# Kernel tuning notes

Measured on AMD Instinct MI355X. Metric: run time of the kernel, lower is better.

## Reference

```python
import jax, jax.numpy as jnp
import numpy as np
from jax import lax

B, C, H, W = 4, 64, 64, 64
CH = C // 2  # edge_detect hidden channels
BN_EPS = 1e-5


def conv1x1(x, w, b):
    # x: (B,C,H,W), w: (O,C), b: (O,)
    return jnp.einsum('bchw,oc->bohw', x, w) + b[None, :, None, None]


def setup_inputs() -> dict:
    key = jax.random.key(0)
    ks = jax.random.split(key, 12)
    s = 1.0 / np.sqrt(C)
    inp = {
        'x': jax.random.normal(ks[0], (B, C, H, W), jnp.float32),
        'Wq': jax.random.normal(ks[1], (C, C), jnp.float32) * s,
        'bq': jnp.zeros((C,), jnp.float32),
        'Wk': jax.random.normal(ks[2], (C, C), jnp.float32) * s,
        'bk': jnp.zeros((C,), jnp.float32),
        'Wv': jax.random.normal(ks[3], (C, C), jnp.float32) * s,
        'bv': jnp.zeros((C,), jnp.float32),
        'We1': jax.random.normal(ks[4], (CH, C, 3, 3), jnp.float32) * (1.0 / np.sqrt(C * 9)),
        'be1': jnp.zeros((CH,), jnp.float32),
        'bn_w': jnp.ones((CH,), jnp.float32),
        'bn_b': jnp.zeros((CH,), jnp.float32),
        'bn_mean': jnp.zeros((CH,), jnp.float32),
        'bn_var': jnp.ones((CH,), jnp.float32),
        'We2': jax.random.normal(ks[5], (1, CH), jnp.float32) * (1.0 / np.sqrt(CH)),
        'be2': jnp.zeros((1,), jnp.float32),
        'gamma': jax.random.normal(ks[6], (1,), jnp.float32) * 0.1,
        'beta': jax.random.normal(ks[7], (1,), jnp.float32) * 0.1,
    }
    return inp


def reference(x, Wq, bq, Wk, bk, Wv, bv, We1, be1, bn_w, bn_b, bn_mean, bn_var, We2, be2, gamma, beta):
    b, c, h, w = x.shape
    hw = h * w
    q = conv1x1(x, Wq, bq).reshape(b, c, hw).transpose(0, 2, 1)  # (B,HW,C)
    k = conv1x1(x, Wk, bk).reshape(b, c, hw)                      # (B,C,HW)
    v = conv1x1(x, Wv, bv).reshape(b, c, hw)                      # (B,C,HW)

    energy = jnp.einsum('bnc,bcm->bnm', q, k)                      # (B,HW,HW)
    attention = jax.nn.softmax(energy, axis=-1)

    # edge_detect: 3x3 conv -> BN (eval stats) -> ReLU -> 1x1 conv -> sigmoid
    e = lax.conv_general_dilated(x, We1, (1, 1), 'SAME',
                                 dimension_numbers=('NCHW', 'OIHW', 'NCHW'))
    e = e + be1[None, :, None, None]
    e = (e - bn_mean[None, :, None, None]) * jax.lax.rsqrt(bn_var + BN_EPS)[None, :, None, None]
    e = e * bn_w[None, :, None, None] + bn_b[None, :, None, None]
    e = jax.nn.relu(e)
    e = conv1x1(e, We2, be2)                                       # (B,1,H,W)
    edge = jax.nn.sigmoid(e).reshape(b, 1, hw)                     # (B,1,HW)

    fa = attention * (1.0 + beta[0] * edge)                        # broadcast over query dim
    denom = jnp.maximum(jnp.sum(jnp.abs(fa), axis=2, keepdims=True), 1e-12)
    fa = fa / denom                                                # L1 renorm along keys

    out = jnp.einsum('bcm,bnm->bcn', v, fa).reshape(b, c, h, w)
    return gamma[0] * out + x
```

## Files before the change

### kernel.cpp

```cpp
#include <hip/hip_runtime.h>
#include <hip/hip_bf16.h>

typedef unsigned short u16;
typedef __attribute__((ext_vector_type(8))) __bf16 bf16x8;
typedef __attribute__((ext_vector_type(4))) float f32x4;


#define NSPLIT 4

__device__ __forceinline__ u16 f2bf(float f) {
    unsigned u = __builtin_bit_cast(unsigned, f);
    u += 0x7FFFu + ((u >> 16) & 1u);
    return (u16)(u >> 16);
}
__device__ __forceinline__ float bf2f(u16 v) {
    unsigned u = ((unsigned)v) << 16;
    return __builtin_bit_cast(float, u);
}

__global__ __launch_bounds__(256) void qkv_edge_kernel(
    const float* __restrict__ x,
    const float* __restrict__ Wq, const float* __restrict__ bq,
    const float* __restrict__ Wk, const float* __restrict__ bk,
    const float* __restrict__ Wv, const float* __restrict__ bv,
    const float* __restrict__ We1, const float* __restrict__ be1,
    const float* __restrict__ bn_w, const float* __restrict__ bn_b,
    const float* __restrict__ bn_mean, const float* __restrict__ bn_var,
    const float* __restrict__ We2, const float* __restrict__ be2,
    const float* __restrict__ beta,
    u16* __restrict__ Qt, u16* __restrict__ Kt, u16* __restrict__ Vm,
    float* __restrict__ wkey)
{
    __shared__ __align__(16) u16 sm[33280];
    const int t = threadIdx.x;
    const int wv = t >> 6, lane = t & 63;
    const int quad = lane >> 4, l15 = lane & 15;

    if (blockIdx.x < 256) {
        u16* Wl   = sm;
        u16* xt_s = sm + 13824;
        u16* vt   = sm + 13824 + 4224;
        const int b = blockIdx.x >> 6;
        const int n0 = (blockIdx.x & 63) << 6;

        const float* Wmat[3] = {Wq, Wk, Wv};
#pragma unroll
        for (int m = 0; m < 3; ++m)
#pragma unroll
            for (int i = 0; i < 4; ++i) {
                int u = t + i * 256;
                float4 w4 = *reinterpret_cast<const float4*>(Wmat[m] + u * 4);
                int row = u >> 4, col = (u & 15) * 4;
                uint2 pk;
                pk.x = (unsigned)f2bf(w4.x) | ((unsigned)f2bf(w4.y) << 16);
                pk.y = (unsigned)f2bf(w4.z) | ((unsigned)f2bf(w4.w) << 16);
                *reinterpret_cast<uint2*>(&Wl[(m * 64 + row) * 72 + col]) = pk;
            }
        for (int i = 0; i < 16; ++i) {
            int lin = t + i * 256;
            int c = lin >> 6, nn = lin & 63;
            xt_s[nn * 66 + c] = f2bf(x[(size_t)(b * 64 + c) * 4096 + n0 + nn]);
        }
        __syncthreads();

        bf16x8 bx[2];
#pragma unroll
        for (int h = 0; h < 2; ++h)
            bx[h] = *reinterpret_cast<const bf16x8*>(
                &xt_s[(wv * 16 + l15) * 66 + h * 32 + quad * 8]);

        f32x4 d[3][4];
#pragma unroll
        for (int m = 0; m < 3; ++m)
#pragma unroll
            for (int mt = 0; mt < 4; ++mt) d[m][mt] = (f32x4){0.f, 0.f, 0.f, 0.f};

#pragma unroll
        for (int h = 0; h < 2; ++h)
#pragma unroll
            for (int m = 0; m < 3; ++m)
#pragma unroll
                for (int mt = 0; mt < 4; ++mt) {
                    bf16x8 af = *reinterpret_cast<const bf16x8*>(
                        &Wl[(m * 64 + mt * 16 + l15) * 72 + h * 32 + quad * 8]);
                    d[m][mt] = __builtin_amdgcn_mfma_f32_16x16x32_bf16(af, bx[h], d[m][mt], 0, 0, 0);
                }

        const float* bias[3] = {bq, bk, bv};
        const float L2E = 1.44269504f;
#pragma unroll
        for (int m = 0; m < 3; ++m)
#pragma unroll
            for (int mt = 0; mt < 4; ++mt) {
                float4 bi = *reinterpret_cast<const float4*>(bias[m] + mt * 16 + quad * 4);
                d[m][mt][0] += bi.x; d[m][mt][1] += bi.y; d[m][mt][2] += bi.z; d[m][mt][3] += bi.w;
                if (m == 0) {
                    d[m][mt][0] *= L2E; d[m][mt][1] *= L2E;
                    d[m][mt][2] *= L2E; d[m][mt][3] *= L2E;
                }
            }

        const int rowchunk = (n0 >> 4) + wv;
#pragma unroll
        for (int m = 0; m < 2; ++m) {
            u16* base = (m == 0 ? Qt : Kt) + (size_t)b * 262144;
#pragma unroll
            for (int mt = 0; mt < 4; ++mt) {
                uint2 pk;
                pk.x = (unsigned)f2bf(d[m][mt][0]) | ((unsigned)f2bf(d[m][mt][1]) << 16);
                pk.y = (unsigned)f2bf(d[m][mt][2]) | ((unsigned)f2bf(d[m][mt][3]) << 16);
                *reinterpret_cast<uint2*>(
                    base + ((size_t)(rowchunk * 8 + mt * 2 + (quad >> 1))) * 128 +
                    l15 * 8 + (quad & 1) * 4) = pk;
            }
        }
#pragma unroll
        for (int mt = 0; mt < 4; ++mt)
#pragma unroll
            for (int r = 0; r < 4; ++r)
                vt[(mt * 16 + quad * 4 + r) * 72 + wv * 16 + l15] = f2bf(d[2][mt][r]);
        __syncthreads();
        {
            u16* Vb_st = Vm + (size_t)b * 262144;
            const int kt = n0 >> 6;
#pragma unroll
            for (int i = 0; i < 2; ++i) {
                int unit = t + i * 256;
                int f = unit >> 7, hq = (unit >> 4) & 7, cl = unit & 15;
                const u16* src = &vt[(f * 16 + cl) * 72 + hq * 8];
                uint4 v4 = *reinterpret_cast<const uint4*>(src);
                *reinterpret_cast<uint4*>(
                    Vb_st + ((size_t)((kt * 4 + f) * 8 + hq)) * 128 + cl * 8) = v4;
            }
        }
    } else {
        u16* Ae_s = sm;
        u16* xr_s = sm + 18688;
        const int eb = blockIdx.x - 256;
        const int b = eb >> 6, h = eb & 63;

        if (t < 192) {
            int kh = t / 64, rem = t & 63;
            int col = (rem >> 5) * 65, ci2 = (rem & 31) * 2;
            *reinterpret_cast<unsigned*>(&xr_s[(kh * 66 + col) * 72 + ci2]) = 0u;
        }
#pragma unroll
        for (int i = 0; i < 18; ++i) {
            int u = t + i * 256;
            int ch = u / 144;
            int rem = u - ch * 144;
            int p = rem >> 4, cig = (rem & 15) * 4;
            const float* src = We1 + ch * 576 + cig * 9 + p;
            float a = src[0], b2 = src[9], c2 = src[18], d2 = src[27];
            uint2 pk;
            pk.x = (unsigned)f2bf(a) | ((unsigned)f2bf(b2) << 16);
            pk.y = (unsigned)f2bf(c2) | ((unsigned)f2bf(d2) << 16);
            *reinterpret_cast<uint2*>(&Ae_s[ch * 584 + p * 64 + cig]) = pk;
        }
#pragma unroll
        for (int i = 0; i < 12; ++i) {
            int u = t + i * 256;
            int w = u & 63, cig = (u >> 6) & 15, kh = u >> 10;
            int hs = h + kh - 1;
            float v0 = 0.f, v1 = 0.f, v2 = 0.f, v3 = 0.f;
            if ((unsigned)hs < 64u) {
                const float* src = x + ((size_t)(b * 64 + cig * 4) * 64 + hs) * 64 + w;
                v0 = src[0]; v1 = src[4096]; v2 = src[8192]; v3 = src[12288];
            }
            uint2 pk;
            pk.x = (unsigned)f2bf(v0) | ((unsigned)f2bf(v1) << 16);
            pk.y = (unsigned)f2bf(v2) | ((unsigned)f2bf(v3) << 16);
            *reinterpret_cast<uint2*>(&xr_s[(kh * 66 + w + 1) * 72 + cig * 4]) = pk;
        }
        __syncthreads();

        f32x4 e[2];
        e[0] = (f32x4){0.f, 0.f, 0.f, 0.f};
        e[1] = (f32x4){0.f, 0.f, 0.f, 0.f};
#pragma unroll
        for (int p = 0; p < 9; ++p) {
            const int kh = p / 3, kw = p - kh * 3;
#pragma unroll
            for (int half = 0; half < 2; ++half) {
                bf16x8 bfr = *reinterpret_cast<const bf16x8*>(
                    &xr_s[(kh * 66 + wv * 16 + l15 + kw) * 72 + half * 32 + quad * 8]);
#pragma unroll
                for (int mt = 0; mt < 2; ++mt) {
                    bf16x8 af = *reinterpret_cast<const bf16x8*>(
                        &Ae_s[(mt * 16 + l15) * 584 + p * 64 + half * 32 + quad * 8]);
                    e[mt] = __builtin_amdgcn_mfma_f32_16x16x32_bf16(af, bfr, e[mt], 0, 0, 0);
                }
            }
        }
        float partial = 0.f;
#pragma unroll
        for (int mt = 0; mt < 2; ++mt) {
            float4 bw = *reinterpret_cast<const float4*>(bn_w    + mt * 16 + quad * 4);
            float4 bb = *reinterpret_cast<const float4*>(bn_b    + mt * 16 + quad * 4);
            float4 bm = *reinterpret_cast<const float4*>(bn_mean + mt * 16 + quad * 4);
            float4 bv2 = *reinterpret_cast<const float4*>(bn_var + mt * 16 + quad * 4);
            float4 b1 = *reinterpret_cast<const float4*>(be1     + mt * 16 + quad * 4);
            float4 w2 = *reinterpret_cast<const float4*>(We2     + mt * 16 + quad * 4);
            float sc, sh;
            sc = bw.x * rsqrtf(bv2.x + 1e-5f); sh = (b1.x - bm.x) * sc + bb.x;
            partial += fmaxf(e[mt][0] * sc + sh, 0.f) * w2.x;
            sc = bw.y * rsqrtf(bv2.y + 1e-5f); sh = (b1.y - bm.y) * sc + bb.y;
            partial += fmaxf(e[mt][1] * sc + sh, 0.f) * w2.y;
            sc = bw.z * rsqrtf(bv2.z + 1e-5f); sh = (b1.z - bm.z) * sc + bb.z;
            partial += fmaxf(e[mt][2] * sc + sh, 0.f) * w2.z;
            sc = bw.w * rsqrtf(bv2.w + 1e-5f); sh = (b1.w - bm.w) * sc + bb.w;
            partial += fmaxf(e[mt][3] * sc + sh, 0.f) * w2.w;
        }
        partial += __shfl_xor(partial, 16);
        partial += __shfl_xor(partial, 32);
        if (lane < 16) {
            float s = partial + be2[0];
            float sg = 1.f / (1.f + __expf(-s));
            wkey[(size_t)b * 4096 + h * 64 + wv * 16 + lane] = 1.f + beta[0] * sg;
        }
    }
}

__global__ __launch_bounds__(128, 2) void attn_kernel(
    const u16* __restrict__ Qt, const u16* __restrict__ Kt,
    const u16* __restrict__ Vm, const float* __restrict__ wkey,
    u16* __restrict__ O_part, float* __restrict__ l_part)
{
    constexpr int KT_ITERS = 64 / NSPLIT;
    const int t = threadIdx.x;
    const int qi = blockIdx.x / NSPLIT;
    const int split = blockIdx.x % NSPLIT;
    const int b = qi >> 6;
    const int n0 = (qi & 63) << 6;
    const int wv = t >> 6, lane = t & 63;
    const int quad = lane >> 4, l15 = lane & 15;

    const int src0 = ((quad & 1) * 2) * 16 + l15;
    const int src1 = src0 + 16;
    const bool msel = (quad >> 1) != 0;

    const u16* Qb = Qt + (size_t)b * 262144;
    const u16* Kb = Kt + (size_t)b * 262144;
    const u16* Vb = Vm + (size_t)b * 262144;
    const float* wb = wkey + (size_t)b * 4096;

    bf16x8 qf[2][2];
#pragma unroll
    for (int nt = 0; nt < 2; ++nt)
#pragma unroll
        for (int h = 0; h < 2; ++h)
            qf[nt][h] = __builtin_bit_cast(bf16x8, *reinterpret_cast<const uint4*>(
                Qb + ((size_t)(((n0 >> 4) + wv * 2 + nt) * 8 + h * 4 + quad)) * 128 + l15 * 8));

    const int kt0 = split * KT_ITERS;
    uint4 kf[4][2];
    float4 wf[4];
#pragma unroll
    for (int mt = 0; mt < 4; ++mt) {
#pragma unroll
        for (int h = 0; h < 2; ++h)
            kf[mt][h] = *reinterpret_cast<const uint4*>(
                Kb + ((size_t)((kt0 * 4 + mt) * 8 + h * 4 + quad)) * 128 + l15 * 8);
        wf[mt] = *reinterpret_cast<const float4*>(wb + kt0 * 64 + mt * 16 + quad * 4);
    }

    const uint4 ones_u = {0x3F803F80u, 0x3F803F80u, 0x3F803F80u, 0x3F803F80u};
    const bf16x8 onesf = __builtin_bit_cast(bf16x8, ones_u);

    f32x4 o[4][2];
    f32x4 l5[2];
#pragma unroll
    for (int fc = 0; fc < 4; ++fc)
#pragma unroll
        for (int nt = 0; nt < 2; ++nt) o[fc][nt] = (f32x4){0.f, 0.f, 0.f, 0.f};
#pragma unroll
    for (int nt = 0; nt < 2; ++nt) l5[nt] = (f32x4){0.f, 0.f, 0.f, 0.f};

    for (int kt = kt0; kt < kt0 + KT_ITERS; ++kt) {
        uint4 vf[4][2];
#pragma unroll
        for (int f = 0; f < 4; ++f)
#pragma unroll
            for (int h = 0; h < 2; ++h)
                vf[f][h] = *reinterpret_cast<const uint4*>(
                    Vb + ((size_t)((kt * 4 + f) * 8 + h * 4 + quad)) * 128 + l15 * 8);

        f32x4 s[4][2];
#pragma unroll
        for (int mt = 0; mt < 4; ++mt)
#pragma unroll
            for (int nt = 0; nt < 2; ++nt) {
                f32x4 a = (f32x4){0.f, 0.f, 0.f, 0.f};
                a = __builtin_amdgcn_mfma_f32_16x16x32_bf16(
                        __builtin_bit_cast(bf16x8, kf[mt][0]), qf[nt][0], a, 0, 0, 0);
                a = __builtin_amdgcn_mfma_f32_16x16x32_bf16(
                        __builtin_bit_cast(bf16x8, kf[mt][1]), qf[nt][1], a, 0, 0, 0);
                s[mt][nt] = a;
            }

        const int ktn = (kt + 1 < kt0 + KT_ITERS) ? kt + 1 : kt0;
#pragma unroll
        for (int mt = 0; mt < 4; ++mt)
#pragma unroll
            for (int h = 0; h < 2; ++h)
                kf[mt][h] = *reinterpret_cast<const uint4*>(
                    Kb + ((size_t)((ktn * 4 + mt) * 8 + h * 4 + quad)) * 128 + l15 * 8);

        uint2 pk[4][2];
        const float OFF = 17.3123405f;
#pragma unroll
        for (int mt = 0; mt < 4; ++mt) {
            const float* wfp = reinterpret_cast<const float*>(&wf[mt]);
#pragma unroll
            for (int nt = 0; nt < 2; ++nt) {
                float p0 = exp2f(s[mt][nt][0] - OFF) * wfp[0];
                float p1 = exp2f(s[mt][nt][1] - OFF) * wfp[1];
                float p2 = exp2f(s[mt][nt][2] - OFF) * wfp[2];
                float p3 = exp2f(s[mt][nt][3] - OFF) * wfp[3];
                unsigned u0 = __builtin_bit_cast(unsigned, p0);
                unsigned u1 = __builtin_bit_cast(unsigned, p1);
                unsigned u2 = __builtin_bit_cast(unsigned, p2);
                unsigned u3 = __builtin_bit_cast(unsigned, p3);
                pk[mt][nt].x = (u0 >> 16) | (u1 & 0xFFFF0000u);
                pk[mt][nt].y = (u2 >> 16) | (u3 & 0xFFFF0000u);
            }
        }

#pragma unroll
        for (int mt = 0; mt < 4; ++mt)
            wf[mt] = *reinterpret_cast<const float4*>(wb + ktn * 64 + mt * 16 + quad * 4);

        bf16x8 pb[2][2];
#pragma unroll
        for (int h = 0; h < 2; ++h)
#pragma unroll
            for (int nt = 0; nt < 2; ++nt) {
                unsigned a0x = (unsigned)__shfl((int)pk[h * 2][nt].x, src0, 64);
                unsigned a1x = (unsigned)__shfl((int)pk[h * 2 + 1][nt].x, src0, 64);
                unsigned a0y = (unsigned)__shfl((int)pk[h * 2][nt].y, src0, 64);
                unsigned a1y = (unsigned)__shfl((int)pk[h * 2 + 1][nt].y, src0, 64);
                unsigned a0z = (unsigned)__shfl((int)pk[h * 2][nt].x, src1, 64);
                unsigned a1z = (unsigned)__shfl((int)pk[h * 2 + 1][nt].x, src1, 64);
                unsigned a0w = (unsigned)__shfl((int)pk[h * 2][nt].y, src1, 64);
                unsigned a1w = (unsigned)__shfl((int)pk[h * 2 + 1][nt].y, src1, 64);
                uint4 g;
                g.x = msel ? a1x : a0x;
                g.y = msel ? a1y : a0y;
                g.z = msel ? a1z : a0z;
                g.w = msel ? a1w : a0w;
                pb[nt][h] = __builtin_bit_cast(bf16x8, g);
            }

#pragma unroll
        for (int nt = 0; nt < 2; ++nt) {
#pragma unroll
            for (int fc = 0; fc < 4; ++fc) {
                o[fc][nt] = __builtin_amdgcn_mfma_f32_16x16x32_bf16(
                    __builtin_bit_cast(bf16x8, vf[fc][0]), pb[nt][0], o[fc][nt], 0, 0, 0);
                o[fc][nt] = __builtin_amdgcn_mfma_f32_16x16x32_bf16(
                    __builtin_bit_cast(bf16x8, vf[fc][1]), pb[nt][1], o[fc][nt], 0, 0, 0);
            }
            l5[nt] = __builtin_amdgcn_mfma_f32_16x16x32_bf16(onesf, pb[nt][0], l5[nt], 0, 0, 0);
            l5[nt] = __builtin_amdgcn_mfma_f32_16x16x32_bf16(onesf, pb[nt][1], l5[nt], 0, 0, 0);
        }
    }

    const size_t pbase = (size_t)blockIdx.x * 4096;
#pragma unroll
    for (int nt = 0; nt < 2; ++nt) {
        if (quad == 0)
            l_part[(size_t)blockIdx.x * 64 + wv * 32 + nt * 16 + l15] = l5[nt][0];
#pragma unroll
        for (int fc = 0; fc < 4; ++fc) {
            uint2 pk2;
            pk2.x = (unsigned)f2bf(o[fc][nt][0]) | ((unsigned)f2bf(o[fc][nt][1]) << 16);
            pk2.y = (unsigned)f2bf(o[fc][nt][2]) | ((unsigned)f2bf(o[fc][nt][3]) << 16);
            *reinterpret_cast<uint2*>(
                &O_part[pbase + ((((wv * 2 + nt) * 4 + fc) * 4 + quad)) * 64 + l15 * 4]) = pk2;
        }
    }
}

__global__ __launch_bounds__(256) void combine_kernel(
    const u16* __restrict__ O_part, const float* __restrict__ l_part,
    const float* __restrict__ x, const float* __restrict__ g_gamma,
    float* __restrict__ out)
{
    __shared__ float ot[16 * 68];
    __shared__ float ls[16];
    const int t = threadIdx.x;
    const int qi = blockIdx.x >> 2;
    const int quarter = blockIdx.x & 3;
    const int b = qi >> 6;
    const int n0 = (qi & 63) << 6;
    const int rbase = (quarter >> 1) * 32 + (quarter & 1) * 16;
    const int f = t >> 6, quad = (t >> 4) & 3, l15 = t & 15;
    const float gamma = g_gamma[0];

    {
        float a0 = 0.f, a1 = 0.f, a2 = 0.f, a3 = 0.f;
#pragma unroll
        for (int s4 = 0; s4 < NSPLIT; ++s4) {
            const u16* base = O_part + ((size_t)(qi * NSPLIT + s4)) * 4096;
            uint2 u = *reinterpret_cast<const uint2*>(
                base + (((quarter * 4 + f) * 4 + quad)) * 64 + l15 * 4);
            a0 += bf2f((u16)(u.x & 0xFFFF));
            a1 += bf2f((u16)(u.x >> 16));
            a2 += bf2f((u16)(u.y & 0xFFFF));
            a3 += bf2f((u16)(u.y >> 16));
        }
        float4 v4; v4.x = a0; v4.y = a1; v4.z = a2; v4.w = a3;
        *reinterpret_cast<float4*>(&ot[l15 * 68 + f * 16 + quad * 4]) = v4;
        if (t < 16) {
            float lsum = 0.f;
#pragma unroll
            for (int s4 = 0; s4 < NSPLIT; ++s4)
                lsum += l_part[((size_t)(qi * NSPLIT + s4)) * 64 + rbase + t];
            ls[t] = gamma / fmaxf(lsum, 1e-30f);
        }
    }
    __syncthreads();
    {
        const int c = t >> 2, nseg = t & 3;
        const size_t gbase = ((size_t)(b * 64 + c)) * 4096 + n0 + rbase + nseg * 4;
        float4 xv = *reinterpret_cast<const float4*>(&x[gbase]);
        float4 rv;
        int nl = nseg * 4;
        rv.x = ot[(nl + 0) * 68 + c] * ls[nl + 0] + xv.x;
        rv.y = ot[(nl + 1) * 68 + c] * ls[nl + 1] + xv.y;
        rv.z = ot[(nl + 2) * 68 + c] * ls[nl + 2] + xv.z;
        rv.w = ot[(nl + 3) * 68 + c] * ls[nl + 3] + xv.w;
        *reinterpret_cast<float4*>(&out[gbase]) = rv;
    }
}

extern "C" void kernel_launch(void* const* d_in, const int* in_sizes, int n_in,
                              void* d_out, int out_size, void* d_ws, size_t ws_size,
                              hipStream_t stream) {
    const float* x      = (const float*)d_in[0];
    const float* Wq     = (const float*)d_in[1];
    const float* bq     = (const float*)d_in[2];
    const float* Wk     = (const float*)d_in[3];
    const float* bk     = (const float*)d_in[4];
    const float* Wv     = (const float*)d_in[5];
    const float* bv     = (const float*)d_in[6];
    const float* We1    = (const float*)d_in[7];
    const float* be1    = (const float*)d_in[8];
    const float* bn_w   = (const float*)d_in[9];
    const float* bn_b   = (const float*)d_in[10];
    const float* bn_mean= (const float*)d_in[11];
    const float* bn_var = (const float*)d_in[12];
    const float* We2    = (const float*)d_in[13];
    const float* be2    = (const float*)d_in[14];
    const float* gamma  = (const float*)d_in[15];
    const float* beta   = (const float*)d_in[16];

    char* ws = (char*)d_ws;
    const size_t KB = 1024, MB = 1024 * 1024;
    u16*   Qt     = (u16*)ws;
    u16*   Kt     = (u16*)(ws + 2 * MB);
    u16*   Vm     = (u16*)(ws + 4 * MB);
    float* wkey   = (float*)(ws + 6 * MB);
    float* l_part = (float*)(ws + 6 * MB + 64 * KB);
    u16*   O_part = (u16*)(ws + 6 * MB + 576 * KB);

    float* out = (float*)d_out;

    qkv_edge_kernel<<<dim3(512), dim3(256), 0, stream>>>(
        x, Wq, bq, Wk, bk, Wv, bv, We1, be1, bn_w, bn_b, bn_mean, bn_var,
        We2, be2, beta, Qt, Kt, Vm, wkey);
    attn_kernel<<<dim3(256 * NSPLIT), dim3(128), 0, stream>>>(
        Qt, Kt, Vm, wkey, O_part, l_part);
    combine_kernel<<<dim3(1024), dim3(256), 0, stream>>>(
        O_part, l_part, x, gamma, out);
}
```

Before: 138.8 us.

## Switch attention to 32x32x16 MFMA with log-weight fold and permlane swap

Rewrites the attention kernel around 32x32x16 bf16 MFMA tiles with 256-thread blocks, each covering 128 queries. The edge weight is now stored as log2 with the offset folded in, so the kernel does one add inside exp2 instead of a subtract and a multiply. The row sum is accumulated in scalar registers instead of with an extra ones-MFMA. P is packed with the hardware cvt_pk_bf16 instruction and rearranged with permlane32_swap instead of eight shuffles per fragment. The combine kernel and output layout change to match, with fewer blocks overall and possibly higher register pressure.

Measured after the change: 156.4 us. +12.7%, slower.

```diff
diff --git a/kernel.cpp b/kernel.cpp
--- a/kernel.cpp
+++ b/kernel.cpp
@@ -4,6 +4,7 @@
 typedef unsigned short u16;
 typedef __attribute__((ext_vector_type(8))) __bf16 bf16x8;
 typedef __attribute__((ext_vector_type(4))) float f32x4;
+typedef __attribute__((ext_vector_type(16))) float f32x16;
 
 
 #define NSPLIT 4
@@ -216,169 +217,155 @@
         if (lane < 16) {
             float s = partial + be2[0];
             float sg = 1.f / (1.f + __expf(-s));
-            wkey[(size_t)b * 4096 + h * 64 + wv * 16 + lane] = 1.f + beta[0] * sg;
+            wkey[(size_t)b * 4096 + h * 64 + wv * 16 + lane] =
+                __log2f(fmaxf(1.f + beta[0] * sg, 1e-20f)) - 17.3123405f;
         }
     }
 }
 
-__global__ __launch_bounds__(128, 2) void attn_kernel(
+__global__ __launch_bounds__(256, 2) void attn_kernel(
     const u16* __restrict__ Qt, const u16* __restrict__ Kt,
-    const u16* __restrict__ Vm, const float* __restrict__ wkey,
+    const u16* __restrict__ Vm, const float* __restrict__ lwkey,
     u16* __restrict__ O_part, float* __restrict__ l_part)
 {
     constexpr int KT_ITERS = 64 / NSPLIT;
     const int t = threadIdx.x;
     const int qi = blockIdx.x / NSPLIT;
     const int split = blockIdx.x % NSPLIT;
-    const int b = qi >> 6;
-    const int n0 = (qi & 63) << 6;
+    const int b = qi >> 5;
+    const int n0 = (qi & 31) << 7;
     const int wv = t >> 6, lane = t & 63;
-    const int quad = lane >> 4, l15 = lane & 15;
-
-    const int src0 = ((quad & 1) * 2) * 16 + l15;
-    const int src1 = src0 + 16;
-    const bool msel = (quad >> 1) != 0;
+    const int l31 = lane & 31, hi = lane >> 5;
+    const int i4 = (lane >> 4) & 1, l15 = lane & 15;
 
     const u16* Qb = Qt + (size_t)b * 262144;
     const u16* Kb = Kt + (size_t)b * 262144;
     const u16* Vb = Vm + (size_t)b * 262144;
-    const float* wb = wkey + (size_t)b * 4096;
-
-    bf16x8 qf[2][2];
-#pragma unroll
-    for (int nt = 0; nt < 2; ++nt)
-#pragma unroll
-        for (int h = 0; h < 2; ++h)
-            qf[nt][h] = __builtin_bit_cast(bf16x8, *reinterpret_cast<const uint4*>(
-                Qb + ((size_t)(((n0 >> 4) + wv * 2 + nt) * 8 + h * 4 + quad)) * 128 + l15 * 8));
+    const float* lwb = lwkey + (size_t)b * 4096;
+
+    bf16x8 qf[4];
+#pragma unroll
+    for (int kc = 0; kc < 4; ++kc)
+        qf[kc] = __builtin_bit_cast(bf16x8, *reinterpret_cast<const uint4*>(
+            Qb + (size_t)(((n0 >> 4) + wv * 2 + i4) * 8 + kc * 2 + hi) * 128 + l15 * 8));
 
     const int kt0 = split * KT_ITERS;
-    uint4 kf[4][2];
-    float4 wf[4];
-#pragma unroll
-    for (int mt = 0; mt < 4; ++mt) {
-#pragma unroll
-        for (int h = 0; h < 2; ++h)
-            kf[mt][h] = *reinterpret_cast<const uint4*>(
-                Kb + ((size_t)((kt0 * 4 + mt) * 8 + h * 4 + quad)) * 128 + l15 * 8);
-        wf[mt] = *reinterpret_cast<const float4*>(wb + kt0 * 64 + mt * 16 + quad * 4);
+    uint4 kf[2][4];
+#pragma unroll
+    for (int tl = 0; tl < 2; ++tl)
+#pragma unroll
+        for (int kc = 0; kc < 4; ++kc)
+            kf[tl][kc] = *reinterpret_cast<const uint4*>(
+                Kb + (size_t)((kt0 * 4 + tl * 2 + i4) * 8 + kc * 2 + hi) * 128 + l15 * 8);
+
+    f32x16 o[2];
+#pragma unroll
+    for (int ct = 0; ct < 2; ++ct)
+#pragma unroll
+        for (int i = 0; i < 16; ++i) o[ct][i] = 0.f;
+    float lacc0 = 0.f, lacc1 = 0.f;
+
+    for (int kt = kt0; kt < kt0 + KT_ITERS; ++kt) {
+        uint4 vf[2][4];
+#pragma unroll
+        for (int ct = 0; ct < 2; ++ct)
+#pragma unroll
+            for (int kc = 0; kc < 4; ++kc)
+                vf[ct][kc] = *reinterpret_cast<const uint4*>(
+                    Vb + (size_t)((kt * 4 + ct * 2 + i4) * 8 + kc * 2 + hi) * 128 + l15 * 8);
+
+        float4 lwv[2][4];
+#pragma unroll
+        for (int tl = 0; tl < 2; ++tl)
+#pragma unroll
+            for (int g = 0; g < 4; ++g)
+                lwv[tl][g] = *reinterpret_cast<const float4*>(
+                    lwb + kt * 64 + tl * 32 + g * 8 + hi * 4);
+
+        f32x16 s[2];
+#pragma unroll
+        for (int tl = 0; tl < 2; ++tl) {
+            f32x16 a;
+#pragma unroll
+            for (int i = 0; i < 16; ++i) a[i] = 0.f;
+#pragma unroll
+            for (int kc = 0; kc < 4; ++kc)
+                a = __builtin_amdgcn_mfma_f32_32x32x16_bf16(
+                        __builtin_bit_cast(bf16x8, kf[tl][kc]), qf[kc], a, 0, 0, 0);
+            s[tl] = a;
+        }
+
+        const int ktn = (kt + 1 < kt0 + KT_ITERS) ? kt + 1 : kt0;
+#pragma unroll
+        for (int tl = 0; tl < 2; ++tl)
+#pragma unroll
+            for (int kc = 0; kc < 4; ++kc)
+                kf[tl][kc] = *reinterpret_cast<const uint4*>(
+                    Kb + (size_t)((ktn * 4 + tl * 2 + i4) * 8 + kc * 2 + hi) * 128 + l15 * 8);
+
+        uint4 pb[2][2];
+#pragma unroll
+        for (int tl = 0; tl < 2; ++tl) {
+            float p[16];
+#pragma unroll
+            for (int g = 0; g < 4; ++g) {
+                const float4 lv = lwv[tl][g];
+                p[4 * g + 0] = exp2f(s[tl][4 * g + 0] + lv.x);
+                p[4 * g + 1] = exp2f(s[tl][4 * g + 1] + lv.y);
+                p[4 * g + 2] = exp2f(s[tl][4 * g + 2] + lv.z);
+                p[4 * g + 3] = exp2f(s[tl][4 * g + 3] + lv.w);
+                lacc0 += p[4 * g + 0] + p[4 * g + 1];
+                lacc1 += p[4 * g + 2] + p[4 * g + 3];
+            }
+#pragma unroll
+            for (int kc2 = 0; kc2 < 2; ++kc2) {
+                int a0, a1, b0, b1;
+                asm("v_cvt_pk_bf16_f32 %0, %1, %2" : "=v"(a0) : "v"(p[kc2 * 8 + 0]), "v"(p[kc2 * 8 + 1]));
+                asm("v_cvt_pk_bf16_f32 %0, %1, %2" : "=v"(a1) : "v"(p[kc2 * 8 + 2]), "v"(p[kc2 * 8 + 3]));
+                asm("v_cvt_pk_bf16_f32 %0, %1, %2" : "=v"(b0) : "v"(p[kc2 * 8 + 4]), "v"(p[kc2 * 8 + 5]));
+                asm("v_cvt_pk_bf16_f32 %0, %1, %2" : "=v"(b1) : "v"(p[kc2 * 8 + 6]), "v"(p[kc2 * 8 + 7]));
+                auto swA = __builtin_amdgcn_permlane32_swap(a0, b0, false, false);
+                auto swB = __builtin_amdgcn_permlane32_swap(a1, b1, false, false);
+                uint4 fr;
+                fr.x = (unsigned)swA[0];
+                fr.y = (unsigned)swB[0];
+                fr.z = (unsigned)swA[1];
+                fr.w = (unsigned)swB[1];
+                pb[tl][kc2] = fr;
+            }
+        }
+
+#pragma unroll
+        for (int ct = 0; ct < 2; ++ct)
+#pragma unroll
+            for (int tl = 0; tl < 2; ++tl)
+#pragma unroll
+                for (int kc2 = 0; kc2 < 2; ++kc2)
+                    o[ct] = __builtin_amdgcn_mfma_f32_32x32x16_bf16(
+                        __builtin_bit_cast(bf16x8, vf[ct][tl * 2 + kc2]),
+                        __builtin_bit_cast(bf16x8, pb[tl][kc2]), o[ct], 0, 0, 0);
     }
 
-    const uint4 ones_u = {0x3F803F80u, 0x3F803F80u, 0x3F803F80u, 0x3F803F80u};
-    const bf16x8 onesf = __builtin_bit_cast(bf16x8, ones_u);
-
-    f32x4 o[4][2];
-    f32x4 l5[2];
-#pragma unroll
-    for (int fc = 0; fc < 4; ++fc)
-#pragma unroll
-        for (int nt = 0; nt < 2; ++nt) o[fc][nt] = (f32x4){0.f, 0.f, 0.f, 0.f};
-#pragma unroll
-    for (int nt = 0; nt < 2; ++nt) l5[nt] = (f32x4){0.f, 0.f, 0.f, 0.f};
-
-    for (int kt = kt0; kt < kt0 + KT_ITERS; ++kt) {
-        uint4 vf[4][2];
-#pragma unroll
-        for (int f = 0; f < 4; ++f)
-#pragma unroll
-            for (int h = 0; h < 2; ++h)
-                vf[f][h] = *reinterpret_cast<const uint4*>(
-                    Vb + ((size_t)((kt * 4 + f) * 8 + h * 4 + quad)) * 128 + l15 * 8);
-
-        f32x4 s[4][2];
-#pragma unroll
-        for (int mt = 0; mt < 4; ++mt)
-#pragma unroll
-            for (int nt = 0; nt < 2; ++nt) {
-                f32x4 a = (f32x4){0.f, 0.f, 0.f, 0.f};
-                a = __builtin_amdgcn_mfma_f32_16x16x32_bf16(
-                        __builtin_bit_cast(bf16x8, kf[mt][0]), qf[nt][0], a, 0, 0, 0);
-                a = __builtin_amdgcn_mfma_f32_16x16x32_bf16(
-                        __builtin_bit_cast(bf16x8, kf[mt][1]), qf[nt][1], a, 0, 0, 0);
-                s[mt][nt] = a;
-            }
-
-        const int ktn = (kt + 1 < kt0 + KT_ITERS) ? kt + 1 : kt0;
-#pragma unroll
-        for (int mt = 0; mt < 4; ++mt)
-#pragma unroll
-            for (int h = 0; h < 2; ++h)
-                kf[mt][h] = *reinterpret_cast<const uint4*>(
-                    Kb + ((size_t)((ktn * 4 + mt) * 8 + h * 4 + quad)) * 128 + l15 * 8);
-
-        uint2 pk[4][2];
-        const float OFF = 17.3123405f;
-#pragma unroll
-        for (int mt = 0; mt < 4; ++mt) {
-            const float* wfp = reinterpret_cast<const float*>(&wf[mt]);
-#pragma unroll
-            for (int nt = 0; nt < 2; ++nt) {
-                float p0 = exp2f(s[mt][nt][0] - OFF) * wfp[0];
-                float p1 = exp2f(s[mt][nt][1] - OFF) * wfp[1];
-                float p2 = exp2f(s[mt][nt][2] - OFF) * wfp[2];
-                float p3 = exp2f(s[mt][nt][3] - OFF) * wfp[3];
-                unsigned u0 = __builtin_bit_cast(unsigned, p0);
-                unsigned u1 = __builtin_bit_cast(unsigned, p1);
-                unsigned u2 = __builtin_bit_cast(unsigned, p2);
-                unsigned u3 = __builtin_bit_cast(unsigned, p3);
-                pk[mt][nt].x = (u0 >> 16) | (u1 & 0xFFFF0000u);
-                pk[mt][nt].y = (u2 >> 16) | (u3 & 0xFFFF0000u);
-            }
-        }
-
-#pragma unroll
-        for (int mt = 0; mt < 4; ++mt)
-            wf[mt] = *reinterpret_cast<const float4*>(wb + ktn * 64 + mt * 16 + quad * 4);
-
-        bf16x8 pb[2][2];
-#pragma unroll
-        for (int h = 0; h < 2; ++h)
-#pragma unroll
-            for (int nt = 0; nt < 2; ++nt) {
-                unsigned a0x = (unsigned)__shfl((int)pk[h * 2][nt].x, src0, 64);
-                unsigned a1x = (unsigned)__shfl((int)pk[h * 2 + 1][nt].x, src0, 64);
-                unsigned a0y = (unsigned)__shfl((int)pk[h * 2][nt].y, src0, 64);
-                unsigned a1y = (unsigned)__shfl((int)pk[h * 2 + 1][nt].y, src0, 64);
-                unsigned a0z = (unsigned)__shfl((int)pk[h * 2][nt].x, src1, 64);
-                unsigned a1z = (unsigned)__shfl((int)pk[h * 2 + 1][nt].x, src1, 64);
-                unsigned a0w = (unsigned)__shfl((int)pk[h * 2][nt].y, src1, 64);
-                unsigned a1w = (unsigned)__shfl((int)pk[h * 2 + 1][nt].y, src1, 64);
-                uint4 g;
-                g.x = msel ? a1x : a0x;
-                g.y = msel ? a1y : a0y;
-                g.z = msel ? a1z : a0z;
-                g.w = msel ? a1w : a0w;
-                pb[nt][h] = __builtin_bit_cast(bf16x8, g);
-            }
-
-#pragma unroll
-        for (int nt = 0; nt < 2; ++nt) {
-#pragma unroll
-            for (int fc = 0; fc < 4; ++fc) {
-                o[fc][nt] = __builtin_amdgcn_mfma_f32_16x16x32_bf16(
-                    __builtin_bit_cast(bf16x8, vf[fc][0]), pb[nt][0], o[fc][nt], 0, 0, 0);
-                o[fc][nt] = __builtin_amdgcn_mfma_f32_16x16x32_bf16(
-                    __builtin_bit_cast(bf16x8, vf[fc][1]), pb[nt][1], o[fc][nt], 0, 0, 0);
-            }
-            l5[nt] = __builtin_amdgcn_mfma_f32_16x16x32_bf16(onesf, pb[nt][0], l5[nt], 0, 0, 0);
-            l5[nt] = __builtin_amdgcn_mfma_f32_16x16x32_bf16(onesf, pb[nt][1], l5[nt], 0, 0, 0);
-        }
-    }
-
-    const size_t pbase = (size_t)blockIdx.x * 4096;
-#pragma unroll
-    for (int nt = 0; nt < 2; ++nt) {
-        if (quad == 0)
-            l_part[(size_t)blockIdx.x * 64 + wv * 32 + nt * 16 + l15] = l5[nt][0];
-#pragma unroll
-        for (int fc = 0; fc < 4; ++fc) {
+    float lh = lacc0 + lacc1;
+    float ltot = lh + __shfl_xor(lh, 32);
+    if (lane < 32)
+        l_part[(size_t)blockIdx.x * 128 + wv * 32 + lane] = ltot;
+
+    const size_t pbase = (size_t)blockIdx.x * 8192;
+    const int q = wv * 32 + l31;
+#pragma unroll
+    for (int ct = 0; ct < 2; ++ct)
+#pragma unroll
+        for (int g = 0; g < 4; ++g) {
+            int w0, w1;
+            asm("v_cvt_pk_bf16_f32 %0, %1, %2" : "=v"(w0) : "v"(o[ct][4 * g + 0]), "v"(o[ct][4 * g + 1]));
+            asm("v_cvt_pk_bf16_f32 %0, %1, %2" : "=v"(w1) : "v"(o[ct][4 * g + 2]), "v"(o[ct][4 * g + 3]));
             uint2 pk2;
-            pk2.x = (unsigned)f2bf(o[fc][nt][0]) | ((unsigned)f2bf(o[fc][nt][1]) << 16);
-            pk2.y = (unsigned)f2bf(o[fc][nt][2]) | ((unsigned)f2bf(o[fc][nt][3]) << 16);
+            pk2.x = (unsigned)w0;
+            pk2.y = (unsigned)w1;
             *reinterpret_cast<uint2*>(
-                &O_part[pbase + ((((wv * 2 + nt) * 4 + fc) * 4 + quad)) * 64 + l15 * 4]) = pk2;
-        }
-    }
+                &O_part[pbase + (size_t)(ct * 8 + g * 2 + hi) * 512 + q * 4]) = pk2;
+        }
 }
 
 __global__ __launch_bounds__(256) void combine_kernel(
@@ -386,51 +373,57 @@
     const float* __restrict__ x, const float* __restrict__ g_gamma,
     float* __restrict__ out)
 {
-    __shared__ float ot[16 * 68];
-    __shared__ float ls[16];
+    __shared__ float ot[32 * 65];
+    __shared__ float ls[32];
     const int t = threadIdx.x;
-    const int qi = blockIdx.x >> 2;
-    const int quarter = blockIdx.x & 3;
-    const int b = qi >> 6;
-    const int n0 = (qi & 63) << 6;
-    const int rbase = (quarter >> 1) * 32 + (quarter & 1) * 16;
-    const int f = t >> 6, quad = (t >> 4) & 3, l15 = t & 15;
+    const int ab = blockIdx.x >> 2;
+    const int sub = blockIdx.x & 3;
+    const int b = ab >> 5;
+    const int n0 = (ab & 31) << 7;
     const float gamma = g_gamma[0];
 
-    {
+#pragma unroll
+    for (int i = 0; i < 2; ++i) {
+        int idx = t + i * 256;
+        int c4 = idx >> 5, ql = idx & 31;
         float a0 = 0.f, a1 = 0.f, a2 = 0.f, a3 = 0.f;
 #pragma unroll
         for (int s4 = 0; s4 < NSPLIT; ++s4) {
-            const u16* base = O_part + ((size_t)(qi * NSPLIT + s4)) * 4096;
             uint2 u = *reinterpret_cast<const uint2*>(
-                base + (((quarter * 4 + f) * 4 + quad)) * 64 + l15 * 4);
+                O_part + ((size_t)(ab * NSPLIT + s4)) * 8192 +
+                (size_t)c4 * 512 + (sub * 32 + ql) * 4);
             a0 += bf2f((u16)(u.x & 0xFFFF));
             a1 += bf2f((u16)(u.x >> 16));
             a2 += bf2f((u16)(u.y & 0xFFFF));
             a3 += bf2f((u16)(u.y >> 16));
         }
-        float4 v4; v4.x = a0; v4.y = a1; v4.z = a2; v4.w = a3;
-        *reinterpret_cast<float4*>(&ot[l15 * 68 + f * 16 + quad * 4]) = v4;
-        if (t < 16) {
-            float lsum = 0.f;
-#pragma unroll
-            for (int s4 = 0; s4 < NSPLIT; ++s4)
-                lsum += l_part[((size_t)(qi * NSPLIT + s4)) * 64 + rbase + t];
-            ls[t] = gamma / fmaxf(lsum, 1e-30f);
-        }
+        ot[ql * 65 + c4 * 4 + 0] = a0;
+        ot[ql * 65 + c4 * 4 + 1] = a1;
+        ot[ql * 65 + c4 * 4 + 2] = a2;
+        ot[ql * 65 + c4 * 4 + 3] = a3;
+    }
+    if (t < 32) {
+        float lsum = 0.f;
+#pragma unroll
+        for (int s4 = 0; s4 < NSPLIT; ++s4)
+            lsum += l_part[((size_t)(ab * NSPLIT + s4)) * 128 + sub * 32 + t];
+        ls[t] = gamma / fmaxf(lsum, 1e-30f);
     }
     __syncthreads();
     {
-        const int c = t >> 2, nseg = t & 3;
-        const size_t gbase = ((size_t)(b * 64 + c)) * 4096 + n0 + rbase + nseg * 4;
-        float4 xv = *reinterpret_cast<const float4*>(&x[gbase]);
-        float4 rv;
-        int nl = nseg * 4;
-        rv.x = ot[(nl + 0) * 68 + c] * ls[nl + 0] + xv.x;
-        rv.y = ot[(nl + 1) * 68 + c] * ls[nl + 1] + xv.y;
-        rv.z = ot[(nl + 2) * 68 + c] * ls[nl + 2] + xv.z;
-        rv.w = ot[(nl + 3) * 68 + c] * ls[nl + 3] + xv.w;
-        *reinterpret_cast<float4*>(&out[gbase]) = rv;
+        const int c = t >> 2, seg = t & 3;
+        const size_t gbase = ((size_t)(b * 64 + c)) * 4096 + n0 + sub * 32 + seg * 8;
+#pragma unroll
+        for (int j = 0; j < 2; ++j) {
+            float4 xv = *reinterpret_cast<const float4*>(&x[gbase + j * 4]);
+            float4 rv;
+            int nl = seg * 8 + j * 4;
+            rv.x = ot[(nl + 0) * 65 + c] * ls[nl + 0] + xv.x;
+            rv.y = ot[(nl + 1) * 65 + c] * ls[nl + 1] + xv.y;
+            rv.z = ot[(nl + 2) * 65 + c] * ls[nl + 2] + xv.z;
+            rv.w = ot[(nl + 3) * 65 + c] * ls[nl + 3] + xv.w;
+            *reinterpret_cast<float4*>(&out[gbase + j * 4]) = rv;
+        }
     }
 }
 
@@ -460,7 +453,7 @@
     u16*   Qt     = (u16*)ws;
     u16*   Kt     = (u16*)(ws + 2 * MB);
     u16*   Vm     = (u16*)(ws + 4 * MB);
-    float* wkey   = (float*)(ws + 6 * MB);
+    float* lw     = (float*)(ws + 6 * MB);
     float* l_part = (float*)(ws + 6 * MB + 64 * KB);
     u16*   O_part = (u16*)(ws + 6 * MB + 576 * KB);
 
@@ -468,9 +461,9 @@
 
     qkv_edge_kernel<<<dim3(512), dim3(256), 0, stream>>>(
         x, Wq, bq, Wk, bk, Wv, bv, We1, be1, bn_w, bn_b, bn_mean, bn_var,
-        We2, be2, beta, Qt, Kt, Vm, wkey);
-    attn_kernel<<<dim3(256 * NSPLIT), dim3(128), 0, stream>>>(
-        Qt, Kt, Vm, wkey, O_part, l_part);
-    combine_kernel<<<dim3(1024), dim3(256), 0, stream>>>(
+        We2, be2, beta, Qt, Kt, Vm, lw);
+    attn_kernel<<<dim3(128 * NSPLIT), dim3(256), 0, stream>>>(
+        Qt, Kt, Vm, lw, O_part, l_part);
+    combine_kernel<<<dim3(512), dim3(256), 0, stream>>>(
         O_part, l_part, x, gamma, out);
 }
```
